# Kernel optimization log

Hardware: AMD Instinct MI355X
Metric: run time of the kernel (lower is better)

## Reference

```python
import jax, jax.numpy as jnp
import numpy as np

B, QL, KL, D, H = 2, 2048, 2048, 1024, 16
E = D // H  # head dim


def setup_inputs() -> dict:
    key = jax.random.key(0)
    ks = jax.random.split(key, 12)
    query_features = jax.random.normal(ks[0], (B, QL, D), dtype=jnp.float32)
    key_features = jax.random.normal(ks[1], (B, KL, D), dtype=jnp.float32)
    # causal additive mask [QL, KL]: -inf above the diagonal, 0 elsewhere
    dependency_mask = jnp.where(
        jnp.arange(KL)[None, :] > jnp.arange(QL)[:, None], -jnp.inf, 0.0
    ).astype(jnp.float32)
    # key padding: random valid lengths in [KL//2, KL]; True = padded position
    lengths = jax.random.randint(ks[2], (B,), KL // 2, KL + 1)
    key_padding_mask = jnp.arange(KL)[None, :] >= lengths[:, None]
    s = 0.02
    Wq = jax.random.normal(ks[3], (D, D), jnp.float32) * s
    bq = jax.random.normal(ks[4], (D,), jnp.float32) * s
    Wk = jax.random.normal(ks[5], (D, D), jnp.float32) * s
    bk = jax.random.normal(ks[6], (D,), jnp.float32) * s
    Wv = jax.random.normal(ks[7], (D, D), jnp.float32) * s
    bv = jax.random.normal(ks[8], (D,), jnp.float32) * s
    Wo = jax.random.normal(ks[9], (D, D), jnp.float32) * s
    bo = jax.random.normal(ks[10], (D,), jnp.float32) * s
    return dict(query_features=query_features, key_features=key_features,
                dependency_mask=dependency_mask, key_padding_mask=key_padding_mask,
                Wq=Wq, bq=bq, Wk=Wk, bk=bk, Wv=Wv, bv=bv, Wo=Wo, bo=bo)


def reference(query_features, key_features, dependency_mask, key_padding_mask,
              Wq, bq, Wk, bk, Wv, bv, Wo, bo):
    b, kl, d = key_features.shape
    ql = query_features.shape[1]
    q = query_features @ Wq.T + bq          # [B, QL, D]
    k = key_features @ Wk.T + bk            # [B, KL, D]
    v = key_features @ Wv.T + bv            # [B, KL, D]
    qh = q.reshape(b, ql, H, E)
    kh = k.reshape(b, kl, H, E)
    vh = v.reshape(b, kl, H, E)
    # NOTE: original scales by sqrt(d_model), not sqrt(head_dim)
    scores = jnp.einsum('bqhe,bkhe->bhqk', qh, kh) / jnp.sqrt(jnp.float32(d))
    scores = jnp.where(key_padding_mask[:, None, None, :], -jnp.inf, scores)
    scores = scores + dependency_mask  # broadcast [QL,KL] over [B,H,QL,KL]
    probs = jax.nn.softmax(scores, axis=-1)  # dropout is identity in eval mode
    agg = jnp.einsum('bhqk,bkhe->bqhe', probs, vh).reshape(b, ql, d)
    return agg @ Wo.T + bo
```

## Files before the change

### kernel.cpp

```cpp
#include <hip/hip_runtime.h>
#include <hip/hip_bf16.h>


typedef __bf16 bf16x8 __attribute__((ext_vector_type(8)));
typedef float f32x4 __attribute__((ext_vector_type(4)));
typedef unsigned int u32x4 __attribute__((ext_vector_type(4)));
typedef unsigned short u16;
typedef unsigned int u32;

#define GLOBAL_AS __attribute__((address_space(1)))
#define LDS_AS __attribute__((address_space(3)))

static __device__ __forceinline__ u16 f2bf(float f) {
    __hip_bfloat16 h = __float2bfloat16(f);
    return __builtin_bit_cast(u16, h);
}
static __device__ __forceinline__ u32 pack2bf(float a, float b) {
    return (u32)f2bf(a) | ((u32)f2bf(b) << 16);
}
static __device__ __forceinline__ float exp2_hw(float x) {
    return __builtin_amdgcn_exp2f(x);
}

__global__ void cvt_all(const float* __restrict__ wq_f, const float* __restrict__ wk_f,
                        const float* __restrict__ wv_f, const float* __restrict__ wo_f,
                        u16* __restrict__ wq, u16* __restrict__ wk,
                        u16* __restrict__ wv, u16* __restrict__ wo,
                        const int* __restrict__ kpm, int* __restrict__ lens) {
    int blk = blockIdx.x;
    if (blk >= 4096) {
        const int b = blk - 4096, tid = threadIdx.x;
        int cnt = 0;
        #pragma unroll
        for (int i = 0; i < 8; ++i) cnt += (kpm[b * 2048 + i * 256 + tid] == 0) ? 1 : 0;
        #pragma unroll
        for (int off = 32; off; off >>= 1) cnt += __shfl_down(cnt, off);
        __shared__ int wsum[4];
        if ((tid & 63) == 0) wsum[tid >> 6] = cnt;
        __syncthreads();
        if (tid == 0) lens[b] = wsum[0] + wsum[1] + wsum[2] + wsum[3];
        return;
    }
    int wsel = blk >> 10;
    int i = (blk & 1023) * 256 + threadIdx.x;
    const float* s; u16* d;
    if (wsel == 0)      { s = wq_f; d = wq; }
    else if (wsel == 1) { s = wk_f; d = wk; }
    else if (wsel == 2) { s = wv_f; d = wv; }
    else                { s = wo_f; d = wo; }
    float4 v = reinterpret_cast<const float4*>(s)[i];
    ushort4 o;
    o.x = f2bf(v.x); o.y = f2bf(v.y); o.z = f2bf(v.z); o.w = f2bf(v.w);
    reinterpret_cast<ushort4*>(d)[i] = o;
}

template<int OUT_F32, int BM, int BN>
__device__ __forceinline__
void gemm_body(const u16* __restrict__ A, const u16* __restrict__ Bw,
               const float* __restrict__ bias, void* __restrict__ Cout,
               int N, int K, float scale, int bx, int by) {
    constexpr int MREP = BM / 32, NREP = BN / 32;
    constexpr int ACH = BM / 8, TCH = ACH + BN / 8;
    constexpr int CPW = TCH / 4;
    __shared__ __attribute__((aligned(16))) u16 aS[BM * 64];
    __shared__ __attribute__((aligned(16))) u16 bS[BN * 64];
    const int tid = threadIdx.x, wave = tid >> 6, lane = tid & 63;
    const int m0 = by * BM, n0 = bx * BN;
    const int wr = wave >> 1, wc = wave & 1;
    const int fr = lane & 15, fq = lane >> 4;
    const int swz_col = (((lane & 7) ^ (lane >> 3)) * 8);
    const int rsw = (fr & 7) << 3;

    f32x4 acc[MREP][NREP] = {};

    for (int k0 = 0; k0 < K; k0 += 64) {
        #pragma unroll
        for (int i = 0; i < CPW; ++i) {
            int chunk = wave * CPW + i;
            const u16* gsrc; u16* ldst;
            if (chunk < ACH) {
                int row = chunk * 8 + (lane >> 3);
                gsrc = A + (size_t)(m0 + row) * K + k0 + swz_col;
                ldst = aS + chunk * 512;
            } else {
                int row = (chunk - ACH) * 8 + (lane >> 3);
                gsrc = Bw + (size_t)(n0 + row) * K + k0 + swz_col;
                ldst = bS + (chunk - ACH) * 512;
            }
            __builtin_amdgcn_global_load_lds((GLOBAL_AS void*)gsrc,
                                             (LDS_AS void*)ldst, 16, 0, 0);
        }
        __syncthreads();
        bf16x8 af[MREP][2], bfr[NREP][2];
        #pragma unroll
        for (int m = 0; m < MREP; ++m)
            #pragma unroll
            for (int h = 0; h < 2; ++h)
                af[m][h] = *reinterpret_cast<const bf16x8*>(
                    &aS[(wr * (BM / 2) + m * 16 + fr) * 64 + ((h * 32 + fq * 8) ^ rsw)]);
        #pragma unroll
        for (int n = 0; n < NREP; ++n)
            #pragma unroll
            for (int h = 0; h < 2; ++h)
                bfr[n][h] = *reinterpret_cast<const bf16x8*>(
                    &bS[(wc * (BN / 2) + n * 16 + fr) * 64 + ((h * 32 + fq * 8) ^ rsw)]);
        __builtin_amdgcn_s_setprio(1);
        #pragma unroll
        for (int m = 0; m < MREP; ++m)
            #pragma unroll
            for (int n = 0; n < NREP; ++n) {
                acc[m][n] = __builtin_amdgcn_mfma_f32_16x16x32_bf16(af[m][0], bfr[n][0], acc[m][n], 0, 0, 0);
                acc[m][n] = __builtin_amdgcn_mfma_f32_16x16x32_bf16(af[m][1], bfr[n][1], acc[m][n], 0, 0, 0);
            }
        __builtin_amdgcn_s_setprio(0);
        __syncthreads();
    }

    #pragma unroll
    for (int n = 0; n < NREP; ++n) {
        int col = n0 + wc * (BN / 2) + n * 16 + fr;
        float bv = bias[col];
        #pragma unroll
        for (int m = 0; m < MREP; ++m) {
            #pragma unroll
            for (int j = 0; j < 4; ++j) {
                int row = m0 + wr * (BM / 2) + m * 16 + fq * 4 + j;
                float v = (acc[m][n][j] + bv) * scale;
                if (OUT_F32)
                    reinterpret_cast<float*>(Cout)[(size_t)row * N + col] = v;
                else
                    reinterpret_cast<u16*>(Cout)[(size_t)row * N + col] = f2bf(v);
            }
        }
    }
}

__global__ __launch_bounds__(256, 3)
void gemm_qkv(const float* __restrict__ xq_f, const float* __restrict__ xk_f,
              const u16* __restrict__ wq, const u16* __restrict__ wk,
              const u16* __restrict__ wv,
              const float* __restrict__ bq, const float* __restrict__ bk,
              const float* __restrict__ bv,
              u16* __restrict__ qb, u16* __restrict__ kb, u16* __restrict__ vb) {
    const int id = blockIdx.x;
    const int g = id & 7, s = id >> 3;
    const int z = s >> 5;
    const int xl = (s >> 3) & 3, byl = s & 7;
    const int bx = (g & 1) * 4 + xl;
    const int by = (g >> 1) * 8 + byl;
    const float* Af = (z == 0) ? xq_f : xk_f;
    const u16* W = (z == 0) ? wq : (z == 1) ? wk : wv;
    const float* bias = (z == 0) ? bq : (z == 1) ? bk : bv;
    u16* C = (z == 0) ? qb : (z == 1) ? kb : vb;
    const float scale = (z == 0) ? 0.0450842200f : 1.0f;

    __shared__ __attribute__((aligned(16))) u16 aS[128 * 64];
    __shared__ __attribute__((aligned(16))) u16 bS[128 * 64];
    const int tid = threadIdx.x, wave = tid >> 6, lane = tid & 63;
    const int m0 = by * 128, n0 = bx * 128;
    const int wr = wave >> 1, wc = wave & 1;
    const int fr = lane & 15, fq = lane >> 4;
    const int r8 = lane >> 3, cb = lane & 7;
    const int swz_col = ((cb ^ r8) * 8);
    const int rsw = (fr & 7) << 3;

    f32x4 acc[4][4] = {};

    for (int k0 = 0; k0 < 1024; k0 += 64) {
        #pragma unroll
        for (int i = 0; i < 4; ++i) {
            int chunk = wave * 4 + i;
            const u16* gsrc = W + (size_t)(n0 + chunk * 8 + r8) * 1024 + k0 + swz_col;
            __builtin_amdgcn_global_load_lds((GLOBAL_AS void*)gsrc,
                                             (LDS_AS void*)(bS + chunk * 512), 16, 0, 0);
        }
        #pragma unroll
        for (int i = 0; i < 4; ++i) {
            int chunk = wave * 4 + i;
            const float* af = Af + (size_t)(m0 + chunk * 8 + r8) * 1024 + k0 + swz_col;
            float4 a0 = reinterpret_cast<const float4*>(af)[0];
            float4 a1 = reinterpret_cast<const float4*>(af)[1];
            u32x4 w;
            w[0] = pack2bf(a0.x, a0.y); w[1] = pack2bf(a0.z, a0.w);
            w[2] = pack2bf(a1.x, a1.y); w[3] = pack2bf(a1.z, a1.w);
            *reinterpret_cast<u32x4*>(aS + chunk * 512 + lane * 8) = w;
        }
        __syncthreads();
        bf16x8 af2[4][2], bfr[4][2];
        #pragma unroll
        for (int m = 0; m < 4; ++m)
            #pragma unroll
            for (int h = 0; h < 2; ++h)
                af2[m][h] = *reinterpret_cast<const bf16x8*>(
                    &aS[(wr * 64 + m * 16 + fr) * 64 + ((h * 32 + fq * 8) ^ rsw)]);
        #pragma unroll
        for (int n = 0; n < 4; ++n)
            #pragma unroll
            for (int h = 0; h < 2; ++h)
                bfr[n][h] = *reinterpret_cast<const bf16x8*>(
                    &bS[(wc * 64 + n * 16 + fr) * 64 + ((h * 32 + fq * 8) ^ rsw)]);
        __builtin_amdgcn_s_setprio(1);
        #pragma unroll
        for (int m = 0; m < 4; ++m)
            #pragma unroll
            for (int n = 0; n < 4; ++n) {
                acc[m][n] = __builtin_amdgcn_mfma_f32_16x16x32_bf16(af2[m][0], bfr[n][0], acc[m][n], 0, 0, 0);
                acc[m][n] = __builtin_amdgcn_mfma_f32_16x16x32_bf16(af2[m][1], bfr[n][1], acc[m][n], 0, 0, 0);
            }
        __builtin_amdgcn_s_setprio(0);
        __syncthreads();
    }

    #pragma unroll
    for (int n = 0; n < 4; ++n) {
        int col = n0 + wc * 64 + n * 16 + fr;
        float bv = bias[col];
        #pragma unroll
        for (int m = 0; m < 4; ++m) {
            #pragma unroll
            for (int j = 0; j < 4; ++j) {
                int row = m0 + wr * 64 + m * 16 + fq * 4 + j;
                float v = (acc[m][n][j] + bv) * scale;
                C[(size_t)row * 1024 + col] = f2bf(v);
            }
        }
    }
}

__global__ __launch_bounds__(256, 2)
void gemm_out(const u16* __restrict__ A, const u16* __restrict__ Bw,
              const float* __restrict__ bias, float* __restrict__ Cout) {
    const int id = blockIdx.x;
    const int g = id & 7, s = id >> 3;
    const int xl = s & 3, byl = s >> 2;
    const int bx = (g & 1) * 4 + xl;
    const int by = (g >> 1) * 16 + byl;
    gemm_body<1, 64, 128>(A, Bw, bias, Cout, 1024, 1024, 1.0f, bx, by);
}

__global__ __launch_bounds__(256, 4)
void attn_fwd(const u16* __restrict__ Qb, const u16* __restrict__ Kb,
              const u16* __restrict__ Vb, const int* __restrict__ lens,
              u16* __restrict__ Ob) {
    __shared__ __attribute__((aligned(16))) u16 Ks[2][64 * 64];
    __shared__ __attribute__((aligned(16))) u16 Vts[2][64 * 64];
    const int tid = threadIdx.x, wave = tid >> 6, lane = tid & 63;
    const int id = blockIdx.x;
    const int bh = (id & 7) * 4 + ((id >> 3) & 3);
    const int k5 = id >> 5;
    const int g = k5 >> 3, x8 = k5 & 7;
    const int qt = (g == 0) ? x8 : (g == 1) ? 31 - x8 : (g == 2) ? 16 + x8 : 15 - x8;
    const int b = bh >> 4, h = bh & 15;
    const int fr = lane & 15, fq = lane >> 4;
    const int t = wave >> 1;
    const int u = wave & 1;
    const int qbase = qt * 64 + u * 32;
    const int len = lens[b];
    const int nt = min(qt + 1, (len + 63) >> 6);

    bf16x8 qa[2][2];
    #pragma unroll
    for (int gq = 0; gq < 2; ++gq) {
        const size_t qoff = (size_t)(b * 2048 + qbase + gq * 16 + fr) * 1024 + h * 64 + fq * 8;
        qa[gq][0] = *reinterpret_cast<const bf16x8*>(Qb + qoff);
        qa[gq][1] = *reinterpret_cast<const bf16x8*>(Qb + qoff + 32);
    }

    bf16x8 ones;
    #pragma unroll
    for (int i = 0; i < 8; ++i) ones[i] = __builtin_bit_cast(__bf16, (u16)0x3F80);

    f32x4 o_acc[2][4] = {};
    f32x4 lacc[2] = {};

    const int e8 = tid >> 5;
    const int c2 = tid & 31;
    const int kp = 2 * c2;
    const int vhalf = kp >> 5, r5 = kp & 31;
    const int fqv = r5 >> 3, nv = (r5 >> 2) & 1, jv = r5 & 3;
    const int k_src = vhalf * 32 + nv * 16 + fqv * 4 + jv;
    const int kswz_col = (((lane & 7) ^ (lane >> 3)) * 8);

    auto issue_K = [&](int kt, int buf) {
        #pragma unroll
        for (int i = 0; i < 2; ++i) {
            int chunk = wave * 2 + i;
            int krow = chunk * 8 + (lane >> 3);
            const u16* gk = Kb + (size_t)(b * 2048 + kt * 64 + krow) * 1024 + h * 64 + kswz_col;
            __builtin_amdgcn_global_load_lds((GLOBAL_AS void*)gk,
                                             (LDS_AS void*)(&Ks[buf][chunk * 512]), 16, 0, 0);
        }
    };
    auto load_V = [&](int kt, ushort4* r) {
        const u16* b1 = Vb + (size_t)(b * 2048 + kt * 64 + k_src) * 1024 + h * 64 + e8 * 8;
        r[0] = reinterpret_cast<const ushort4*>(b1)[0];
        r[1] = reinterpret_cast<const ushort4*>(b1 + 4)[0];
        r[2] = reinterpret_cast<const ushort4*>(b1 + 1024)[0];
        r[3] = reinterpret_cast<const ushort4*>(b1 + 1024 + 4)[0];
    };
    auto write_V = [&](const ushort4* r, int buf) {
        u32* vbase = reinterpret_cast<u32*>(&Vts[buf][0]);
        const u16* lo16 = reinterpret_cast<const u16*>(&r[0]);
        const u16* hi16 = reinterpret_cast<const u16*>(&r[2]);
        #pragma unroll
        for (int i = 0; i < 8; ++i) {
            u32 w = (u32)lo16[i] | ((u32)hi16[i] << 16);
            vbase[(e8 * 8 + i) * 32 + (c2 ^ (i << 2))] = w;
        }
    };

    {
        ushort4 vr[4];
        issue_K(0, 0);
        load_V(0, vr);
        write_V(vr, 0);
    }
    __syncthreads();

    for (int kt = 0; kt < nt; ++kt) {
        const int k0 = kt * 64;
        const int kbase = k0 + t * 32;
        const int cur = kt & 1, nxt = cur ^ 1;
        const bool has_next = (kt + 1 < nt);

        ushort4 vr[4];
        if (has_next) {
            issue_K(kt + 1, nxt);
            load_V(kt + 1, vr);
        }

        f32x4 s[2][2] = {};
        __builtin_amdgcn_s_setprio(1);
        #pragma unroll
        for (int kq2 = 0; kq2 < 2; ++kq2) {
            int kr = t * 32 + kq2 * 16 + fr;
            int sw = (fr & 7) << 3;
            bf16x8 kb0 = *reinterpret_cast<const bf16x8*>(&Ks[cur][kr * 64 + ((fq * 8) ^ sw)]);
            bf16x8 kb1 = *reinterpret_cast<const bf16x8*>(&Ks[cur][kr * 64 + ((32 + fq * 8) ^ sw)]);
            #pragma unroll
            for (int gq = 0; gq < 2; ++gq) {
                s[kq2][gq] = __builtin_amdgcn_mfma_f32_16x16x32_bf16(kb0, qa[gq][0], s[kq2][gq], 0, 0, 0);
                s[kq2][gq] = __builtin_amdgcn_mfma_f32_16x16x32_bf16(kb1, qa[gq][1], s[kq2][gq], 0, 0, 0);
            }
        }
        __builtin_amdgcn_s_setprio(0);

        const bool fullt = (kbase + 31 <= qbase) && (kbase + 32 <= len);
        if (!fullt) {
            #pragma unroll
            for (int kq2 = 0; kq2 < 2; ++kq2)
                #pragma unroll
                for (int gq = 0; gq < 2; ++gq) {
                    int qg = qbase + gq * 16 + fr;
                    #pragma unroll
                    for (int j = 0; j < 4; ++j) {
                        int kg = kbase + kq2 * 16 + fq * 4 + j;
                        s[kq2][gq][j] = (kg <= qg && kg < len) ? s[kq2][gq][j] : -1e30f;
                    }
                }
        }
        #pragma unroll
        for (int kq2 = 0; kq2 < 2; ++kq2)
            #pragma unroll
            for (int gq = 0; gq < 2; ++gq)
                #pragma unroll
                for (int j = 0; j < 4; ++j)
                    s[kq2][gq][j] = exp2_hw(s[kq2][gq][j]);

        bf16x8 pa[2];
        #pragma unroll
        for (int gq = 0; gq < 2; ++gq) {
            u32x4 w;
            w[0] = pack2bf(s[0][gq][0], s[0][gq][1]);
            w[1] = pack2bf(s[0][gq][2], s[0][gq][3]);
            w[2] = pack2bf(s[1][gq][0], s[1][gq][1]);
            w[3] = pack2bf(s[1][gq][2], s[1][gq][3]);
            pa[gq] = __builtin_bit_cast(bf16x8, w);
        }

        if (has_next) write_V(vr, nxt);

        __builtin_amdgcn_s_setprio(1);
        bf16x8 vbr[4];
        #pragma unroll
        for (int n = 0; n < 4; ++n) {
            int vr2 = n * 16 + fr;
            vbr[n] = *reinterpret_cast<const bf16x8*>(
                &Vts[cur][vr2 * 64 + ((t * 32 + fq * 8) ^ ((fr & 7) << 3))]);
        }
        #pragma unroll
        for (int gq = 0; gq < 2; ++gq) {
            lacc[gq] = __builtin_amdgcn_mfma_f32_16x16x32_bf16(pa[gq], ones, lacc[gq], 0, 0, 0);
            #pragma unroll
            for (int n = 0; n < 4; ++n)
                o_acc[gq][n] = __builtin_amdgcn_mfma_f32_16x16x32_bf16(pa[gq], vbr[n], o_acc[gq][n], 0, 0, 0);
        }
        __builtin_amdgcn_s_setprio(0);

        __syncthreads();
    }

    __syncthreads();
    float* ocomb = reinterpret_cast<float*>(&Ks[0][0]);
    float* lcomb = reinterpret_cast<float*>(&Vts[0][0]);
    if (t == 1) {
        #pragma unroll
        for (int gq = 0; gq < 2; ++gq)
            #pragma unroll
            for (int j = 0; j < 4; ++j) {
                int ql = u * 32 + gq * 16 + fq * 4 + j;
                #pragma unroll
                for (int n = 0; n < 4; ++n)
                    ocomb[ql * 64 + n * 16 + fr] = o_acc[gq][n][j];
                if (fr == 0) lcomb[ql] = lacc[gq][j];
            }
    }
    __syncthreads();
    if (t == 0) {
        #pragma unroll
        for (int gq = 0; gq < 2; ++gq)
            #pragma unroll
            for (int j = 0; j < 4; ++j) {
                int ql = u * 32 + gq * 16 + fq * 4 + j;
                float inv = 1.f / (lacc[gq][j] + lcomb[ql]);
                int row = qt * 64 + ql;
                #pragma unroll
                for (int n = 0; n < 4; ++n) {
                    float osum = o_acc[gq][n][j] + ocomb[ql * 64 + n * 16 + fr];
                    Ob[(size_t)(b * 2048 + row) * 1024 + h * 64 + n * 16 + fr] = f2bf(osum * inv);
                }
            }
    }
}

extern "C" void kernel_launch(void* const* d_in, const int* in_sizes, int n_in,
                              void* d_out, int out_size, void* d_ws, size_t ws_size,
                              hipStream_t stream) {
    const float* xq_f = (const float*)d_in[0];
    const float* xk_f = (const float*)d_in[1];
    const int* kpm = (const int*)d_in[3];
    const float* Wq = (const float*)d_in[4];
    const float* bq = (const float*)d_in[5];
    const float* Wk = (const float*)d_in[6];
    const float* bk = (const float*)d_in[7];
    const float* Wv = (const float*)d_in[8];
    const float* bv = (const float*)d_in[9];
    const float* Wo = (const float*)d_in[10];
    const float* bo = (const float*)d_in[11];

    u16* ws = (u16*)d_ws;
    u16* xq = ws;
    u16* xk = xq + 4194304;
    u16* wq = xk + 4194304;
    u16* wk = wq + 1048576;
    u16* wv = wk + 1048576;
    u16* wo = wv + 1048576;
    u16* qb = wo + 1048576;
    u16* kb2 = qb + 4194304;
    u16* vb2 = kb2 + 4194304;
    u16* ag = vb2 + 4194304;
    int* lens = (int*)(ag + 4194304);

    cvt_all<<<4098, 256, 0, stream>>>(Wq, Wk, Wv, Wo, wq, wk, wv, wo, kpm, lens);

    gemm_qkv<<<768, 256, 0, stream>>>(xq_f, xk_f, wq, wk, wv,
                                      bq, bk, bv, qb, kb2, vb2);

    attn_fwd<<<1024, 256, 0, stream>>>(qb, kb2, vb2, lens, ag);

    gemm_out<<<512, 256, 0, stream>>>(ag, wo, bo, (float*)d_out);
}
```

Before: 100.5 us.

## Double-buffer out-projection GEMM, DMA fp32 activations into LDS for QKV, pad attention combine

The output-projection GEMM body gets double-buffered LDS tiles, so the next K-slab's global-to-LDS loads are issued while the current slab is computed. The QKV GEMM stops loading fp32 activations into registers and converting before the LDS store. It now DMAs fp32 tiles straight into LDS with global_load_lds, using K=32 steps and an XOR swizzle, and converts to bf16 when reading fragments. The attention epilogue pads the cross-wave combine buffer to a row stride of 68 to avoid LDS bank conflicts. The QKV path halves the K-step and so doubles the number of barriers, and its fp32 LDS reads are wider.

```diff
diff --git a/kernel.cpp b/kernel.cpp
--- a/kernel.cpp
+++ b/kernel.cpp
@@ -56,14 +56,14 @@
 
 template<int OUT_F32, int BM, int BN>
 __device__ __forceinline__
-void gemm_body(const u16* __restrict__ A, const u16* __restrict__ Bw,
-               const float* __restrict__ bias, void* __restrict__ Cout,
-               int N, int K, float scale, int bx, int by) {
+void gemm_body_dbuf(const u16* __restrict__ A, const u16* __restrict__ Bw,
+                    const float* __restrict__ bias, void* __restrict__ Cout,
+                    int N, int K, float scale, int bx, int by) {
     constexpr int MREP = BM / 32, NREP = BN / 32;
     constexpr int ACH = BM / 8, TCH = ACH + BN / 8;
     constexpr int CPW = TCH / 4;
-    __shared__ __attribute__((aligned(16))) u16 aS[BM * 64];
-    __shared__ __attribute__((aligned(16))) u16 bS[BN * 64];
+    __shared__ __attribute__((aligned(16))) u16 aS[2][BM * 64];
+    __shared__ __attribute__((aligned(16))) u16 bS[2][BN * 64];
     const int tid = threadIdx.x, wave = tid >> 6, lane = tid & 63;
     const int m0 = by * BM, n0 = bx * BN;
     const int wr = wave >> 1, wc = wave & 1;
@@ -73,7 +73,7 @@
 
     f32x4 acc[MREP][NREP] = {};
 
-    for (int k0 = 0; k0 < K; k0 += 64) {
+    auto stage = [&](int k0, int buf) {
         #pragma unroll
         for (int i = 0; i < CPW; ++i) {
             int chunk = wave * CPW + i;
@@ -81,29 +81,37 @@
             if (chunk < ACH) {
                 int row = chunk * 8 + (lane >> 3);
                 gsrc = A + (size_t)(m0 + row) * K + k0 + swz_col;
-                ldst = aS + chunk * 512;
+                ldst = &aS[buf][chunk * 512];
             } else {
                 int row = (chunk - ACH) * 8 + (lane >> 3);
                 gsrc = Bw + (size_t)(n0 + row) * K + k0 + swz_col;
-                ldst = bS + (chunk - ACH) * 512;
+                ldst = &bS[buf][(chunk - ACH) * 512];
             }
             __builtin_amdgcn_global_load_lds((GLOBAL_AS void*)gsrc,
                                              (LDS_AS void*)ldst, 16, 0, 0);
         }
-        __syncthreads();
+    };
+
+    stage(0, 0);
+    __syncthreads();
+    int cur = 0;
+
+    for (int k0 = 0; k0 < K; k0 += 64) {
+        if (k0 + 64 < K) stage(k0 + 64, cur ^ 1);
+
         bf16x8 af[MREP][2], bfr[NREP][2];
         #pragma unroll
         for (int m = 0; m < MREP; ++m)
             #pragma unroll
             for (int h = 0; h < 2; ++h)
                 af[m][h] = *reinterpret_cast<const bf16x8*>(
-                    &aS[(wr * (BM / 2) + m * 16 + fr) * 64 + ((h * 32 + fq * 8) ^ rsw)]);
+                    &aS[cur][(wr * (BM / 2) + m * 16 + fr) * 64 + ((h * 32 + fq * 8) ^ rsw)]);
         #pragma unroll
         for (int n = 0; n < NREP; ++n)
             #pragma unroll
             for (int h = 0; h < 2; ++h)
                 bfr[n][h] = *reinterpret_cast<const bf16x8*>(
-                    &bS[(wc * (BN / 2) + n * 16 + fr) * 64 + ((h * 32 + fq * 8) ^ rsw)]);
+                    &bS[cur][(wc * (BN / 2) + n * 16 + fr) * 64 + ((h * 32 + fq * 8) ^ rsw)]);
         __builtin_amdgcn_s_setprio(1);
         #pragma unroll
         for (int m = 0; m < MREP; ++m)
@@ -114,6 +122,7 @@
             }
         __builtin_amdgcn_s_setprio(0);
         __syncthreads();
+        cur ^= 1;
     }
 
     #pragma unroll
@@ -154,59 +163,61 @@
     u16* C = (z == 0) ? qb : (z == 1) ? kb : vb;
     const float scale = (z == 0) ? 0.0450842200f : 1.0f;
 
-    __shared__ __attribute__((aligned(16))) u16 aS[128 * 64];
-    __shared__ __attribute__((aligned(16))) u16 bS[128 * 64];
+    __shared__ __attribute__((aligned(16))) float aSf[128 * 32];
+    __shared__ __attribute__((aligned(16))) u16 bS[128 * 32];
     const int tid = threadIdx.x, wave = tid >> 6, lane = tid & 63;
     const int m0 = by * 128, n0 = bx * 128;
     const int wr = wave >> 1, wc = wave & 1;
     const int fr = lane & 15, fq = lane >> 4;
-    const int r8 = lane >> 3, cb = lane & 7;
-    const int swz_col = ((cb ^ r8) * 8);
-    const int rsw = (fr & 7) << 3;
+    const int a_sub = lane >> 3, a_g = lane & 7;
+    const int b_sub = lane >> 2, b_g = lane & 3;
 
     f32x4 acc[4][4] = {};
 
-    for (int k0 = 0; k0 < 1024; k0 += 64) {
-        #pragma unroll
-        for (int i = 0; i < 4; ++i) {
-            int chunk = wave * 4 + i;
-            const u16* gsrc = W + (size_t)(n0 + chunk * 8 + r8) * 1024 + k0 + swz_col;
-            __builtin_amdgcn_global_load_lds((GLOBAL_AS void*)gsrc,
-                                             (LDS_AS void*)(bS + chunk * 512), 16, 0, 0);
-        }
-        #pragma unroll
-        for (int i = 0; i < 4; ++i) {
-            int chunk = wave * 4 + i;
-            const float* af = Af + (size_t)(m0 + chunk * 8 + r8) * 1024 + k0 + swz_col;
-            float4 a0 = reinterpret_cast<const float4*>(af)[0];
-            float4 a1 = reinterpret_cast<const float4*>(af)[1];
+    for (int k0 = 0; k0 < 1024; k0 += 32) {
+        #pragma unroll
+        for (int i = 0; i < 6; ++i) {
+            int chunk = wave * 6 + i;
+            if (chunk < 16) {
+                int row = chunk * 8 + a_sub;
+                const float* gsrc = Af + (size_t)(m0 + row) * 1024 + k0 + ((a_g ^ (row & 7)) * 4);
+                __builtin_amdgcn_global_load_lds((GLOBAL_AS void*)gsrc,
+                    (LDS_AS void*)(aSf + chunk * 256 + lane * 4), 16, 0, 0);
+            } else {
+                int bc = chunk - 16;
+                int row = bc * 16 + b_sub;
+                const u16* gsrc = W + (size_t)(n0 + row) * 1024 + k0 + ((b_g ^ ((row >> 2) & 3)) * 8);
+                __builtin_amdgcn_global_load_lds((GLOBAL_AS void*)gsrc,
+                    (LDS_AS void*)(bS + bc * 512 + lane * 8), 16, 0, 0);
+            }
+        }
+        __syncthreads();
+
+        bf16x8 af[4];
+        #pragma unroll
+        for (int m = 0; m < 4; ++m) {
+            int row = wr * 64 + m * 16 + fr;
+            int r7 = row & 7;
+            f32x4 a0 = *reinterpret_cast<const f32x4*>(&aSf[row * 32 + (((2 * fq) ^ r7) * 4)]);
+            f32x4 a1 = *reinterpret_cast<const f32x4*>(&aSf[row * 32 + (((2 * fq + 1) ^ r7) * 4)]);
             u32x4 w;
-            w[0] = pack2bf(a0.x, a0.y); w[1] = pack2bf(a0.z, a0.w);
-            w[2] = pack2bf(a1.x, a1.y); w[3] = pack2bf(a1.z, a1.w);
-            *reinterpret_cast<u32x4*>(aS + chunk * 512 + lane * 8) = w;
-        }
-        __syncthreads();
-        bf16x8 af2[4][2], bfr[4][2];
+            w[0] = pack2bf(a0[0], a0[1]); w[1] = pack2bf(a0[2], a0[3]);
+            w[2] = pack2bf(a1[0], a1[1]); w[3] = pack2bf(a1[2], a1[3]);
+            af[m] = __builtin_bit_cast(bf16x8, w);
+        }
+        bf16x8 bfr[4];
+        #pragma unroll
+        for (int n = 0; n < 4; ++n) {
+            int row = wc * 64 + n * 16 + fr;
+            bfr[n] = *reinterpret_cast<const bf16x8*>(
+                &bS[row * 32 + ((fq ^ ((row >> 2) & 3)) * 8)]);
+        }
+        __builtin_amdgcn_s_setprio(1);
         #pragma unroll
         for (int m = 0; m < 4; ++m)
             #pragma unroll
-            for (int h = 0; h < 2; ++h)
-                af2[m][h] = *reinterpret_cast<const bf16x8*>(
-                    &aS[(wr * 64 + m * 16 + fr) * 64 + ((h * 32 + fq * 8) ^ rsw)]);
-        #pragma unroll
-        for (int n = 0; n < 4; ++n)
-            #pragma unroll
-            for (int h = 0; h < 2; ++h)
-                bfr[n][h] = *reinterpret_cast<const bf16x8*>(
-                    &bS[(wc * 64 + n * 16 + fr) * 64 + ((h * 32 + fq * 8) ^ rsw)]);
-        __builtin_amdgcn_s_setprio(1);
-        #pragma unroll
-        for (int m = 0; m < 4; ++m)
-            #pragma unroll
-            for (int n = 0; n < 4; ++n) {
-                acc[m][n] = __builtin_amdgcn_mfma_f32_16x16x32_bf16(af2[m][0], bfr[n][0], acc[m][n], 0, 0, 0);
-                acc[m][n] = __builtin_amdgcn_mfma_f32_16x16x32_bf16(af2[m][1], bfr[n][1], acc[m][n], 0, 0, 0);
-            }
+            for (int n = 0; n < 4; ++n)
+                acc[m][n] = __builtin_amdgcn_mfma_f32_16x16x32_bf16(af[m], bfr[n], acc[m][n], 0, 0, 0);
         __builtin_amdgcn_s_setprio(0);
         __syncthreads();
     }
@@ -235,7 +246,7 @@
     const int xl = s & 3, byl = s >> 2;
     const int bx = (g & 1) * 4 + xl;
     const int by = (g >> 1) * 16 + byl;
-    gemm_body<1, 64, 128>(A, Bw, bias, Cout, 1024, 1024, 1.0f, bx, by);
+    gemm_body_dbuf<1, 64, 128>(A, Bw, bias, Cout, 1024, 1024, 1.0f, bx, by);
 }
 
 __global__ __launch_bounds__(256, 4)
@@ -402,7 +413,7 @@
 
     __syncthreads();
     float* ocomb = reinterpret_cast<float*>(&Ks[0][0]);
-    float* lcomb = reinterpret_cast<float*>(&Vts[0][0]);
+    float* lcomb = ocomb + 64 * 68;
     if (t == 1) {
         #pragma unroll
         for (int gq = 0; gq < 2; ++gq)
@@ -411,7 +422,7 @@
                 int ql = u * 32 + gq * 16 + fq * 4 + j;
                 #pragma unroll
                 for (int n = 0; n < 4; ++n)
-                    ocomb[ql * 64 + n * 16 + fr] = o_acc[gq][n][j];
+                    ocomb[ql * 68 + n * 16 + fr] = o_acc[gq][n][j];
                 if (fr == 0) lcomb[ql] = lacc[gq][j];
             }
     }
@@ -426,7 +437,7 @@
                 int row = qt * 64 + ql;
                 #pragma unroll
                 for (int n = 0; n < 4; ++n) {
-                    float osum = o_acc[gq][n][j] + ocomb[ql * 64 + n * 16 + fr];
+                    float osum = o_acc[gq][n][j] + ocomb[ql * 68 + n * 16 + fr];
                     Ob[(size_t)(b * 2048 + row) * 1024 + h * 64 + n * 16 + fr] = f2bf(osum * inv);
                 }
             }
```

After: 106.1 us. 5.6% more time.
